# Optimization experiments

Measured on AMD Instinct MI355X. Metric: run time of the kernel, lower is better.

The kernel has to match this reference:

```python
import jax, jax.numpy as jnp
import numpy as np

BLOCK = 9      # photometric_loss block size
LOSS_EPS = 0.5 # census ternary threshold


def _sign_eps(d, eps):
    # ternary census: -1 / 0 / +1 with dead-zone eps
    return jnp.where(d < -eps, -1.0, jnp.where(d > eps, 1.0, 0.0))


def _census_sad(es, ta, block, eps):
    # per-pixel mean over valid 9x9 window of |census(es) - census(ta)|
    B, C, H, W = es.shape
    P = block // 2
    pad = ((0, 0), (0, 0), (P, P), (P, P))
    esp = jnp.pad(es, pad)
    tap = jnp.pad(ta, pad)
    vp = jnp.pad(jnp.ones((1, 1, H, W), es.dtype), pad)  # validity of shifted px
    total = jnp.zeros_like(es)
    count = jnp.zeros((1, 1, H, W), es.dtype)
    for dh in range(-P, P + 1):          # fixed 9x9 structural loop
        for dw in range(-P, P + 1):
            es_s = esp[:, :, P + dh:P + dh + H, P + dw:P + dw + W]
            ta_s = tap[:, :, P + dh:P + dh + H, P + dw:P + dw + W]
            v = vp[:, :, P + dh:P + dh + H, P + dw:P + dw + W]
            c = jnp.abs(_sign_eps(es_s - es, eps) - _sign_eps(ta_s - ta, eps))
            total = total + v * c
            count = count + v
    return total / count


def reference(disp0, im, pattern):
    B, _, H, W = disp0.shape
    # pattern.mean(dim=1, keepdim=True)
    pat = jnp.broadcast_to(pattern.mean(axis=1, keepdims=True), (B, 1, H, W))
    # grid_sample(align_corners=True, border) with y unchanged reduces to
    # clamped 1D linear interpolation along width at x = u - disp
    u = jnp.arange(W, dtype=disp0.dtype)
    x = jnp.clip(u[None, None, None, :] - disp0, 0.0, W - 1)  # [B,1,H,W]
    x0 = jnp.floor(x).astype(jnp.int32)
    x1 = jnp.minimum(x0 + 1, W - 1)
    w = x - x0.astype(x.dtype)
    p0 = jnp.take_along_axis(pat, x0, axis=3)
    p1 = jnp.take_along_axis(pat, x1, axis=3)
    pattern_proj = p0 * (1.0 - w) + p1 * w
    diff = _census_sad(pattern_proj, im, BLOCK, LOSS_EPS)
    # mask = ones (std=None): (mask*diff).sum()/mask.sum() == mean
    val = diff.mean()
    return val, pattern_proj


def setup_inputs() -> dict:
    key = jax.random.key(0)
    k1, k2, k3 = jax.random.split(key, 3)
    B, H, W = 16, 512, 640
    disp0 = jax.random.uniform(k1, (B, 1, H, W), dtype=jnp.float32) * 64.0
    im = jax.random.uniform(k2, (B, 1, H, W), dtype=jnp.float32)
    pattern = jax.random.uniform(k3, (1, 3, H, W), dtype=jnp.float32)
    return {"disp0": disp0, "im": im, "pattern": pattern}
```

## Files before the change

### kernel.cpp

```cpp
#include <hip/hip_runtime.h>

#define BB 16
#define HH 512
#define WW 640
constexpr int HW = HH * WW;
constexpr float BIGF = 1.0e6f;

#define WT 64
#define HT 32
#define RP 8
#define PAD 4
#define LW (WT + 2*PAD)
#define LH (HT + 2*PAD)

__global__ __launch_bounds__(256)
void fused_kernel(const float* __restrict__ disp0,
                  const float* __restrict__ im,
                  const float* __restrict__ pattern,
                  float* __restrict__ out)
{
    __shared__ float es_t[LH * LW];
    __shared__ float ta_t[LH * LW];
    __shared__ float wsum[4];

    const int bx = blockIdx.x, by = blockIdx.y, b = blockIdx.z;
    const int tx = threadIdx.x;
    const int rg = threadIdx.y;
    const int tid = rg * 64 + tx;

    const float* db = disp0 + (size_t)b * HW;
    const float* ib = im    + (size_t)b * HW;
    float* proj = out + 1 + (size_t)b * HW;

    const int gh0 = by * HT - PAD;
    const int gw0 = bx * WT - PAD;

    #pragma unroll
    for (int it = 0; it < (LH * LW + 255) / 256; ++it) {
        int i = tid + it * 256;
        if (i < LH * LW) {
            int lh = i / LW;
            int lw = i - lh * LW;
            int gh = gh0 + lh, gw = gw0 + lw;
            float ev = BIGF, tv = BIGF;
            if ((gh >= 0) & (gh < HH) & (gw >= 0) & (gw < WW)) {
                int g = gh * WW + gw;
                float d = db[g];
                float x = fminf(fmaxf((float)gw - d, 0.0f), (float)(WW - 1));
                int   x0 = (int)x;
                int   x1 = min(x0 + 1, WW - 1);
                float w  = x - (float)x0;
                const float* prow = pattern + gh * WW;
                float p0 = (prow[x0] + prow[HW + x0] + prow[2*HW + x0]) * (1.0f/3.0f);
                float p1 = (prow[x1] + prow[HW + x1] + prow[2*HW + x1]) * (1.0f/3.0f);
                ev = p0 * (1.0f - w) + p1 * w;
                tv = ib[g];
                if ((lh >= PAD) & (lh < PAD + HT) & (lw >= PAD) & (lw < PAD + WT))
                    proj[g] = ev;
            }
            es_t[i] = ev;
            ta_t[i] = tv;
        }
    }
    __syncthreads();

    float ec[RP], tc[RP], acc[RP];
    #pragma unroll
    for (int p = 0; p < RP; ++p) {
        int lr = rg * RP + p + PAD;
        ec[p]  = es_t[lr * LW + tx + PAD];
        tc[p]  = ta_t[lr * LW + tx + PAD];
        acc[p] = 0.0f;
    }

    for (int wr = 0; wr < RP + 2 * PAD; ++wr) {
        int lr = rg * RP + wr;
        float e[9], t[9];
        #pragma unroll
        for (int j = 0; j < 9; ++j) {
            e[j] = es_t[lr * LW + tx + j];
            t[j] = ta_t[lr * LW + tx + j];
        }
        #pragma unroll
        for (int p = 0; p < RP; ++p) {
            if (p >= wr - 2 * PAD && p <= wr) {
                #pragma unroll
                for (int j = 0; j < 9; ++j) {
                    float s1 = rintf(fminf(fmaxf(e[j] - ec[p], -1.0f), 1.0f));
                    float s2 = rintf(fminf(fmaxf(t[j] - tc[p], -1.0f), 1.0f));
                    acc[p] += fabsf(s1 - s2);
                }
            }
        }
    }

    const int w  = bx * WT + tx;
    const int cw = min(PAD, WW - 1 - w) + min(PAD, w) + 1;
    float tsum = 0.0f;
    #pragma unroll
    for (int p = 0; p < RP; ++p) {
        int h  = by * HT + rg * RP + p;
        int ch = min(PAD, HH - 1 - h) + min(PAD, h) + 1;
        tsum += acc[p] / (float)(ch * cw);
    }
    #pragma unroll
    for (int off = 32; off > 0; off >>= 1)
        tsum += __shfl_down(tsum, off, 64);
    if (tx == 0) wsum[rg] = tsum;
    __syncthreads();
    if (tid == 0) {
        float s = (wsum[0] + wsum[1] + wsum[2] + wsum[3]) * (1.0f / ((float)BB * (float)HW));
        atomicAdd(out, s);
    }
}

extern "C" void kernel_launch(void* const* d_in, const int* in_sizes, int n_in,
                              void* d_out, int out_size, void* d_ws, size_t ws_size,
                              hipStream_t stream) {
    const float* disp0   = (const float*)d_in[0];
    const float* im      = (const float*)d_in[1];
    const float* pattern = (const float*)d_in[2];
    float* out = (float*)d_out;

    hipMemsetAsync(d_out, 0, sizeof(float), stream);

    dim3 grid(WW / WT, HH / HT, BB);
    dim3 block(64, 4);
    fused_kernel<<<grid, block, 0, stream>>>(disp0, im, pattern, out);
}
```

Baseline: 173.8 us.

## Exploit census pair symmetry with packed fp16 taps and a two-stage reduction

The census comparison is symmetric, so each pixel pair is evaluated only once over a half window (4 taps in the centre row plus 4 rows below), and the interior sum is doubled. Edge pixels carry per-pair weights built from reciprocals of the valid-window counts. Projected-pattern and image values are packed into one fp16x2 shared tile, which halves LDS traffic and lets both ternary signs come from one packed clamp-and-round sequence. Interior tiles take a cheaper unweighted fp16 accumulate path, and the memset plus global atomic is replaced by per-block partials summed in a second kernel. The fp16 inputs and fp16 accumulation risk small accuracy differences near the threshold and in the sums.

```diff
diff --git a/kernel.cpp b/kernel.cpp
--- a/kernel.cpp
+++ b/kernel.cpp
@@ -4,23 +4,111 @@
 #define HH 512
 #define WW 640
 constexpr int HW = HH * WW;
-constexpr float BIGF = 1.0e6f;
 
 #define WT 64
 #define HT 32
-#define RP 8
 #define PAD 4
 #define LW (WT + 2*PAD)
-#define LH (HT + 2*PAD)
+#define LH (HT + PAD)
+#define GX (WW / WT)
+#define GY (HH / HT)
+#define NBLK (GX * GY * BB)
+
+typedef _Float16 h2 __attribute__((ext_vector_type(2)));
+
+constexpr float HALO = 30000.0f;
+
+__device__ __forceinline__ float fast_rcp(float x) {
+#if __has_builtin(__builtin_amdgcn_rcpf)
+    return __builtin_amdgcn_rcpf(x);
+#else
+    return 1.0f / x;
+#endif
+}
+
+__device__ __forceinline__ _Float16 habs(_Float16 x) {
+    union { _Float16 h; unsigned short u; } v;
+    v.h = x; v.u &= 0x7fffu;
+    return v.h;
+}
+
+template<bool EDGE>
+__device__ __forceinline__ float census_sum(const h2* sm, int tx, int rg,
+                                            int bx, int by)
+{
+    const h2 K2   = { (_Float16)1536.0f, (_Float16)1536.0f };
+    const h2 ONE2 = { (_Float16)1.0f,  (_Float16)1.0f };
+    const h2 NEG2 = { (_Float16)-1.0f, (_Float16)-1.0f };
+
+    float invcw[9];
+    if constexpr (EDGE) {
+        int w0 = bx * WT + tx;
+        #pragma unroll
+        for (int j = 0; j < 9; ++j) {
+            int c  = w0 + j - 4;
+            int cw = min(4, WW - 1 - c) + min(4, c) + 1;
+            invcw[j] = fast_rcp((float)cw);
+        }
+    }
+
+    float tsum = 0.0f;
+    #pragma unroll 1
+    for (int p = 0; p < 8; ++p) {
+        const int lr = rg * 8 + p;
+        const h2* base = sm + lr * LW + tx;
+        const h2 ct = base[PAD];
+
+        float invch[5], wp;
+        float facc = 0.0f;
+        _Float16 hacc = (_Float16)0.0f;
+        if constexpr (EDGE) {
+            int r0 = by * HT + lr;
+            #pragma unroll
+            for (int d = 0; d < 5; ++d) {
+                int r  = r0 + d;
+                int ch = min(4, HH - 1 - r) + min(4, r) + 1;
+                invch[d] = fast_rcp((float)ch);
+            }
+            wp = invch[0] * invcw[4];
+        }
+
+        auto tap = [&](int dh, int j) {
+            h2 d2 = base[dh * LW + j] - ct;
+            d2 = __builtin_elementwise_max(d2, NEG2);
+            d2 = __builtin_elementwise_min(d2, ONE2);
+            d2 = d2 + K2;
+            d2 = d2 - K2;
+            _Float16 diff = d2.x - d2.y;
+            if constexpr (EDGE) {
+                float c  = fabsf((float)diff);
+                float wt = fmaf(invch[dh], invcw[j], wp);
+                facc = fmaf(c, wt, facc);
+            } else {
+                hacc = hacc + habs(diff);
+            }
+        };
+
+        #pragma unroll
+        for (int j = 5; j <= 8; ++j) tap(0, j);
+        #pragma unroll
+        for (int dh = 1; dh <= 4; ++dh) {
+            #pragma unroll
+            for (int j = 0; j <= 8; ++j) tap(dh, j);
+        }
+
+        tsum += EDGE ? facc : (float)hacc;
+    }
+    return tsum;
+}
 
 __global__ __launch_bounds__(256)
 void fused_kernel(const float* __restrict__ disp0,
                   const float* __restrict__ im,
                   const float* __restrict__ pattern,
-                  float* __restrict__ out)
+                  float* __restrict__ out,
+                  float* __restrict__ partial)
 {
-    __shared__ float es_t[LH * LW];
-    __shared__ float ta_t[LH * LW];
+    __shared__ h2 sm[LH * LW];
     __shared__ float wsum[4];
 
     const int bx = blockIdx.x, by = blockIdx.y, b = blockIdx.z;
@@ -32,7 +120,7 @@
     const float* ib = im    + (size_t)b * HW;
     float* proj = out + 1 + (size_t)b * HW;
 
-    const int gh0 = by * HT - PAD;
+    const int gh0 = by * HT;
     const int gw0 = bx * WT - PAD;
 
     #pragma unroll
@@ -42,8 +130,8 @@
             int lh = i / LW;
             int lw = i - lh * LW;
             int gh = gh0 + lh, gw = gw0 + lw;
-            float ev = BIGF, tv = BIGF;
-            if ((gh >= 0) & (gh < HH) & (gw >= 0) & (gw < WW)) {
+            float ev = HALO, tv = HALO;
+            if ((gh < HH) & (gw >= 0) & (gw < WW)) {
                 int g = gh * WW + gw;
                 float d = db[g];
                 float x = fminf(fmaxf((float)gw - d, 0.0f), (float)(WW - 1));
@@ -55,63 +143,46 @@
                 float p1 = (prow[x1] + prow[HW + x1] + prow[2*HW + x1]) * (1.0f/3.0f);
                 ev = p0 * (1.0f - w) + p1 * w;
                 tv = ib[g];
-                if ((lh >= PAD) & (lh < PAD + HT) & (lw >= PAD) & (lw < PAD + WT))
+                if ((lh < HT) & (lw >= PAD) & (lw < PAD + WT))
                     proj[g] = ev;
             }
-            es_t[i] = ev;
-            ta_t[i] = tv;
+            h2 pk = { (_Float16)ev, (_Float16)tv };
+            sm[i] = pk;
         }
     }
     __syncthreads();
 
-    float ec[RP], tc[RP], acc[RP];
-    #pragma unroll
-    for (int p = 0; p < RP; ++p) {
-        int lr = rg * RP + p + PAD;
-        ec[p]  = es_t[lr * LW + tx + PAD];
-        tc[p]  = ta_t[lr * LW + tx + PAD];
-        acc[p] = 0.0f;
-    }
-
-    for (int wr = 0; wr < RP + 2 * PAD; ++wr) {
-        int lr = rg * RP + wr;
-        float e[9], t[9];
-        #pragma unroll
-        for (int j = 0; j < 9; ++j) {
-            e[j] = es_t[lr * LW + tx + j];
-            t[j] = ta_t[lr * LW + tx + j];
-        }
-        #pragma unroll
-        for (int p = 0; p < RP; ++p) {
-            if (p >= wr - 2 * PAD && p <= wr) {
-                #pragma unroll
-                for (int j = 0; j < 9; ++j) {
-                    float s1 = rintf(fminf(fmaxf(e[j] - ec[p], -1.0f), 1.0f));
-                    float s2 = rintf(fminf(fmaxf(t[j] - tc[p], -1.0f), 1.0f));
-                    acc[p] += fabsf(s1 - s2);
-                }
-            }
-        }
-    }
-
-    const int w  = bx * WT + tx;
-    const int cw = min(PAD, WW - 1 - w) + min(PAD, w) + 1;
-    float tsum = 0.0f;
-    #pragma unroll
-    for (int p = 0; p < RP; ++p) {
-        int h  = by * HT + rg * RP + p;
-        int ch = min(PAD, HH - 1 - h) + min(PAD, h) + 1;
-        tsum += acc[p] / (float)(ch * cw);
-    }
+    float tsum;
+    if ((bx >= 1) & (bx <= GX - 2) & (by >= 1) & (by <= GY - 2)) {
+        tsum = census_sum<false>(sm, tx, rg, bx, by) * (2.0f / 81.0f);
+    } else {
+        tsum = census_sum<true>(sm, tx, rg, bx, by);
+    }
+
     #pragma unroll
     for (int off = 32; off > 0; off >>= 1)
         tsum += __shfl_down(tsum, off, 64);
     if (tx == 0) wsum[rg] = tsum;
     __syncthreads();
-    if (tid == 0) {
-        float s = (wsum[0] + wsum[1] + wsum[2] + wsum[3]) * (1.0f / ((float)BB * (float)HW));
-        atomicAdd(out, s);
-    }
+    if (tid == 0)
+        partial[(b * GY + by) * GX + bx] = wsum[0] + wsum[1] + wsum[2] + wsum[3];
+}
+
+__global__ __launch_bounds__(256)
+void reduce_kernel(const float* __restrict__ partial, float* __restrict__ out)
+{
+    __shared__ float wsum[4];
+    int t = threadIdx.x;
+    float s = 0.0f;
+    #pragma unroll
+    for (int i = 0; i < NBLK / 256; ++i) s += partial[t + i * 256];
+    #pragma unroll
+    for (int off = 32; off > 0; off >>= 1)
+        s += __shfl_down(s, off, 64);
+    if ((t & 63) == 0) wsum[t >> 6] = s;
+    __syncthreads();
+    if (t == 0)
+        out[0] = (wsum[0] + wsum[1] + wsum[2] + wsum[3]) * (1.0f / ((float)BB * (float)HW));
 }
 
 extern "C" void kernel_launch(void* const* d_in, const int* in_sizes, int n_in,
@@ -121,10 +192,10 @@
     const float* im      = (const float*)d_in[1];
     const float* pattern = (const float*)d_in[2];
     float* out = (float*)d_out;
-
-    hipMemsetAsync(d_out, 0, sizeof(float), stream);
-
-    dim3 grid(WW / WT, HH / HT, BB);
+    float* partial = (float*)d_ws;
+
+    dim3 grid(GX, GY, BB);
     dim3 block(64, 4);
-    fused_kernel<<<grid, block, 0, stream>>>(disp0, im, pattern, out);
-}
+    fused_kernel<<<grid, block, 0, stream>>>(disp0, im, pattern, out, partial);
+    reduce_kernel<<<1, 256, 0, stream>>>(partial, out);
+}
```

New measurement: 158.9 us. -8.6%, faster.
